# Optimization experiments

Hardware: AMD Instinct MI355X
Metric: run time of the kernel (lower is better)

The kernel has to match this reference:

```python
import jax, jax.numpy as jnp
import numpy as np

NUM_HEADS = 16

def setup_inputs() -> dict:
    key = jax.random.key(0)
    ks = jax.random.split(key, 6)
    B, S, D = 2, 2048, 1024
    x = jax.random.normal(ks[0], (B, S, D), dtype=jnp.float32)
    s = 1.0 / np.sqrt(D)
    Wq = jax.random.normal(ks[1], (D, D), dtype=jnp.float32) * s
    Wk = jax.random.normal(ks[2], (D, D), dtype=jnp.float32) * s
    Wv = jax.random.normal(ks[3], (D, D), dtype=jnp.float32) * s
    Wff = jax.random.normal(ks[4], (D, D), dtype=jnp.float32) * s
    bff = jax.random.normal(ks[5], (D,), dtype=jnp.float32) * 0.01
    return {"x": x, "Wq": Wq, "Wk": Wk, "Wv": Wv, "Wff": Wff, "bff": bff}

def reference(x, Wq, Wk, Wv, Wff, bff):
    B, S, D = x.shape
    H = NUM_HEADS
    Dh = D // H
    # Q/K/V projections (bias-free Linears). Original scales Q by 1/sqrt(hidden_size).
    q = (x @ Wq.T) * (1.0 / jnp.sqrt(jnp.asarray(D, x.dtype)))
    k = x @ Wk.T
    v = x @ Wv.T
    q = q.reshape(B, S, H, Dh)
    k = k.reshape(B, S, H, Dh)
    v = v.reshape(B, S, H, Dh)
    # Blockwise online-softmax attention is mathematically identical to
    # full softmax attention over all keys (no causal mask in source).
    scores = jnp.einsum('bqhd,bkhd->bhqk', q, k)
    attn = jax.nn.softmax(scores, axis=-1)
    out = jnp.einsum('bhqk,bkhd->bqhd', attn, v).reshape(B, S, D)
    # Final feedforward Linear(hidden, hidden) with bias.
    return out @ Wff.T + bff
```

## Files before the change

### kernel.cpp

```cpp
#include <hip/hip_runtime.h>
#include <stdint.h>

typedef __attribute__((ext_vector_type(8))) short bf16x8;
typedef __attribute__((ext_vector_type(4))) float f32x4;

__device__ __forceinline__ uint16_t f2bf(float f) {
  union { float f; uint32_t u; } a; a.f = f;
  uint32_t u = a.u;
  u += 0x7FFFu + ((u >> 16) & 1u);
  return (uint16_t)(u >> 16);
}

__device__ __forceinline__ uint32_t pk_bf16(float a, float b) {
#if __has_builtin(__builtin_amdgcn_cvt_pk_bf16_f32)
  auto r = __builtin_amdgcn_cvt_pk_bf16_f32(a, b);
  uint32_t u; __builtin_memcpy(&u, &r, sizeof(u));
  return u;
#else
  return (uint32_t)f2bf(a) | ((uint32_t)f2bf(b) << 16);
#endif
}

__device__ __forceinline__ uint32_t pk_bf16_fast(float a, float b) {
#if __has_builtin(__builtin_amdgcn_cvt_pk_bf16_f32)
  auto r = __builtin_amdgcn_cvt_pk_bf16_f32(a, b);
  uint32_t u; __builtin_memcpy(&u, &r, sizeof(u));
  return u;
#else
  uint32_t ua, ub;
  __builtin_memcpy(&ua, &a, 4); __builtin_memcpy(&ub, &b, 4);
  return __builtin_amdgcn_perm(ub, ua, 0x07060302u);
#endif
}

__device__ __forceinline__ float fast_exp2(float x) {
#if __has_builtin(__builtin_amdgcn_exp2f)
  return __builtin_amdgcn_exp2f(x);
#else
  return exp2f(x);
#endif
}

__device__ __forceinline__ void gld_lds16(const uint16_t* g, uint16_t* l) {
  __builtin_amdgcn_global_load_lds(
      (const __attribute__((address_space(1))) void*)g,
      (__attribute__((address_space(3))) void*)l, 16, 0, 0);
}

__global__ void cast_all(const float* __restrict__ x, const float* __restrict__ wq,
                         const float* __restrict__ wk, const float* __restrict__ wv,
                         const float* __restrict__ wff,
                         uint16_t* __restrict__ xb, uint16_t* __restrict__ wqb,
                         uint16_t* __restrict__ wkb, uint16_t* __restrict__ wvb,
                         uint16_t* __restrict__ wffb) {
  int i = blockIdx.x * blockDim.x + threadIdx.x;
  const float* src; uint16_t* dst; int off;
  if (i < 1048576)      { src = x;   dst = xb;   off = i; }
  else if (i < 1310720) { src = wq;  dst = wqb;  off = i - 1048576; }
  else if (i < 1572864) { src = wk;  dst = wkb;  off = i - 1310720; }
  else if (i < 1835008) { src = wv;  dst = wvb;  off = i - 1572864; }
  else                  { src = wff; dst = wffb; off = i - 1835008; }
  float4 v = ((const float4*)src)[off];
  uint2 o; o.x = pk_bf16(v.x, v.y); o.y = pk_bf16(v.z, v.w);
  ((uint2*)dst)[off] = o;
}

__device__ __forceinline__ void gemm_tile(const uint16_t* __restrict__ Abase,
                                          const uint16_t* __restrict__ Bbase,
                                          uint16_t* lds, f32x4 acc[4][4]) {
  const int tid  = threadIdx.x;
  const int w    = tid >> 6;
  const int lane = tid & 63;
  const int wm   = w >> 1, wn = w & 1;
  const int lrow = lane & 15;
  const int quad = lane >> 4;
  const int srow = lane >> 3;
  const int lc   = (lane & 7) ^ srow;
  const int sx   = lrow & 7;
  uint16_t* a_lds = lds;
  uint16_t* b_lds = lds + 8192;

#pragma unroll
  for (int mt = 0; mt < 4; ++mt)
#pragma unroll
    for (int nt = 0; nt < 4; ++nt)
      acc[mt][nt] = (f32x4){0.f, 0.f, 0.f, 0.f};

  const uint16_t* ag = Abase + (size_t)(w * 32 + srow) * 1024 + lc * 8;
  const uint16_t* bg = Bbase + (size_t)(w * 32 + srow) * 1024 + lc * 8;

  for (int k0 = 0; k0 < 1024; k0 += 64) {
#pragma unroll
    for (int i8 = 0; i8 < 4; ++i8) {
      gld_lds16(ag + (size_t)i8 * 8 * 1024 + k0, a_lds + (w * 4 + i8) * 512);
      gld_lds16(bg + (size_t)i8 * 8 * 1024 + k0, b_lds + (w * 4 + i8) * 512);
    }
    __syncthreads();
#pragma unroll
    for (int ks = 0; ks < 2; ++ks) {
      bf16x8 af[4], bfr[4];
      const int c = ((ks * 4 + quad) ^ sx) << 3;
#pragma unroll
      for (int mt = 0; mt < 4; ++mt)
        af[mt] = *(const bf16x8*)(a_lds + (wm * 64 + mt * 16 + lrow) * 64 + c);
#pragma unroll
      for (int nt = 0; nt < 4; ++nt)
        bfr[nt] = *(const bf16x8*)(b_lds + (wn * 64 + nt * 16 + lrow) * 64 + c);
#pragma unroll
      for (int mt = 0; mt < 4; ++mt)
#pragma unroll
        for (int nt = 0; nt < 4; ++nt)
          acc[mt][nt] = __builtin_amdgcn_mfma_f32_16x16x32_bf16(af[mt], bfr[nt], acc[mt][nt], 0, 0, 0);
    }
    __syncthreads();
  }
}

__global__ __launch_bounds__(256) void gemm_qkv(
    const uint16_t* __restrict__ x,
    const uint16_t* __restrict__ wq, const uint16_t* __restrict__ wk, const uint16_t* __restrict__ wv,
    uint16_t* __restrict__ qo, uint16_t* __restrict__ ko, uint16_t* __restrict__ vto) {
  __shared__ __align__(16) uint16_t lds[17408];
  const int m0 = blockIdx.x * 128, n0 = blockIdx.y * 128, z = blockIdx.z;
  f32x4 acc[4][4];
  if (z < 2) {
    const uint16_t* W = (z == 0) ? wq : wk;
    gemm_tile(W + (size_t)n0 * 1024, x + (size_t)m0 * 1024, lds, acc);
  } else {
    gemm_tile(x + (size_t)m0 * 1024, wv + (size_t)n0 * 1024, lds, acc);
  }

  const int tid = threadIdx.x;
  const int lane = tid & 63, w = tid >> 6;
  const int wm = w >> 1, wn = w & 1, lrow = lane & 15, quad = lane >> 4;
  const float scale = (z == 0) ? 0.045084222f : 1.0f;

#pragma unroll
  for (int mt = 0; mt < 4; ++mt)
#pragma unroll
    for (int nt = 0; nt < 4; ++nt) {
      int i0 = wm * 64 + mt * 16 + quad * 4;
      int j  = wn * 64 + nt * 16 + lrow;
      uint2 dd;
      dd.x = pk_bf16(acc[mt][nt][0] * scale, acc[mt][nt][1] * scale);
      dd.y = pk_bf16(acc[mt][nt][2] * scale, acc[mt][nt][3] * scale);
      *(uint2*)(&lds[j * 136 + i0]) = dd;
    }
  __syncthreads();

  uint16_t* outp = (z == 0) ? qo : (z == 1) ? ko : vto;
  if (z < 2) {
#pragma unroll
    for (int it = 0; it < 8; ++it) {
      int idx = it * 256 + tid;
      int jj = idx >> 4, cc = idx & 15;
      uint4 v = *(const uint4*)(&lds[jj * 136 + cc * 8]);
      int m = m0 + jj, n = n0 + cc * 8;
      int b = m >> 11, s = m & 2047, h = n >> 6, dh = n & 63;
      *(uint4*)(outp + ((size_t)((b * 16 + h) * 2048 + s)) * 64 + dh) = v;
    }
  } else {
    int b = m0 >> 11, sbase = m0 & 2047;
#pragma unroll
    for (int it = 0; it < 8; ++it) {
      int idx = it * 256 + tid;
      int ff = idx >> 4, cc = idx & 15;
      uint4 v = *(const uint4*)(&lds[ff * 136 + cc * 8]);
      int n = n0 + ff, h = n >> 6, dh = n & 63;
      *(uint4*)(outp + ((size_t)((b * 16 + h) * 64 + dh)) * 2048 + sbase + cc * 8) = v;
    }
  }
}

__global__ __launch_bounds__(256) void gemm_ff(
    const uint16_t* __restrict__ ao, const uint16_t* __restrict__ wff,
    const float* __restrict__ bff, float* __restrict__ out) {
  __shared__ __align__(16) uint16_t lds[17408];
  const int m0 = blockIdx.x * 128, n0 = blockIdx.y * 128;
  f32x4 acc[4][4];
  gemm_tile(wff + (size_t)n0 * 1024, ao + (size_t)m0 * 1024, lds, acc);

  const int tid = threadIdx.x;
  const int lane = tid & 63, w = tid >> 6;
  const int wm = w >> 1, wn = w & 1, lrow = lane & 15, quad = lane >> 4;
  float* fl = (float*)lds;

#pragma unroll
  for (int p = 0; p < 2; ++p) {
    if (wm == p) {
#pragma unroll
      for (int mt = 0; mt < 4; ++mt)
#pragma unroll
        for (int nt = 0; nt < 4; ++nt) {
          int i0 = mt * 16 + quad * 4;
          int j  = wn * 64 + nt * 16 + lrow;
          *(f32x4*)(&fl[j * 68 + i0]) = acc[mt][nt];
        }
    }
    __syncthreads();
#pragma unroll
    for (int it = 0; it < 8; ++it) {
      int idx = it * 256 + tid;
      int jj = idx >> 4, cc = idx & 15;
      f32x4 v = *(const f32x4*)(&fl[jj * 68 + cc * 4]);
      int n = n0 + p * 64 + cc * 4;
      f32x4 bias = *(const f32x4*)(bff + n);
      f32x4 vv = v + bias;
      *(f32x4*)(out + (size_t)(m0 + jj) * 1024 + n) = vv;
    }
    __syncthreads();
  }
}

__global__ __launch_bounds__(512, 4) void attn(
    const uint16_t* __restrict__ q, const uint16_t* __restrict__ k,
    const uint16_t* __restrict__ vt, uint16_t* __restrict__ ao) {
  __shared__ __align__(16) uint16_t lds_all[32768];
  uint16_t* const k_lds = lds_all;
  uint16_t* const v_lds = lds_all + 8192;
  uint16_t* const p_lds = lds_all + 16384;
  const int tid = threadIdx.x, w = tid >> 6, lane = tid & 63;
  const int lrow = lane & 15, quad = lane >> 4;
  const int srow = lane >> 3, lc = (lane & 7) ^ srow, sx = lrow & 7;
  const int kw = w & 3, qw = w >> 2;
  const int pk = w & 1, pq = w >> 1;
  const int pswz = (lrow & 7) << 1;

  const int lin = blockIdx.x + (blockIdx.y << 4);
  const int wl  = ((lin & 7) << 6) + (lin >> 3);
  const int qb  = wl & 15, bh = wl >> 4;

  const uint16_t* Q = q  + (size_t)bh * (2048 * 64);
  const uint16_t* K = k  + (size_t)bh * (2048 * 64);
  const uint16_t* V = vt + (size_t)bh * (64 * 2048);

  const int qr0 = qb * 128;
  bf16x8 qf[4][2];
#pragma unroll
  for (int qh = 0; qh < 4; ++qh)
#pragma unroll
    for (int ks = 0; ks < 2; ++ks)
      qf[qh][ks] = *(const bf16x8*)(Q + (size_t)(qr0 + qw * 64 + qh * 16 + lrow) * 64 + ks * 32 + quad * 8);

  f32x4 o[2][4];
#pragma unroll
  for (int qh2 = 0; qh2 < 2; ++qh2)
#pragma unroll
    for (int dt = 0; dt < 4; ++dt) o[qh2][dt] = (f32x4){0.f, 0.f, 0.f, 0.f};
  float ls[4] = {0.f, 0.f, 0.f, 0.f};
  bf16x8 vfr[4];

  auto stage = [&](int kb, int bi) {
    gld_lds16(K + (size_t)(kb * 64 + w * 8 + srow) * 64 + lc * 8, k_lds + bi * 4096 + w * 512);
    gld_lds16(V + (size_t)(w * 8 + srow) * 2048 + kb * 64 + lc * 8, v_lds + bi * 4096 + w * 512);
  };
  stage(0, 0);

  for (int kb = 0; kb < 32; ++kb) {
    const int bi = kb & 1;
    __syncthreads();

    if (kb > 0) {
      const uint16_t* pbuf = p_lds + (bi ^ 1) * 8192;
      __builtin_amdgcn_s_setprio(1);
#pragma unroll
      for (int qh2 = 0; qh2 < 2; ++qh2) {
        int row = pq * 32 + qh2 * 16 + lrow;
        bf16x8 pa = *(const bf16x8*)(pbuf + row * 64 + (((pk * 8 + quad * 2) ^ pswz) << 2));
#pragma unroll
        for (int dt = 0; dt < 4; ++dt)
          o[qh2][dt] = __builtin_amdgcn_mfma_f32_16x16x32_bf16(vfr[dt], pa, o[qh2][dt], 0, 0, 0);
      }
      __builtin_amdgcn_s_setprio(0);
    }

#pragma unroll
    for (int dt = 0; dt < 4; ++dt)
      vfr[dt] = *(const bf16x8*)(v_lds + bi * 4096 + (dt * 16 + lrow) * 64 + (((pk * 4 + quad) ^ sx) << 3));

    if (kb + 1 < 32) stage(kb + 1, bi ^ 1);

    f32x4 s[4];
#pragma unroll
    for (int qh = 0; qh < 4; ++qh) s[qh] = (f32x4){0.f, 0.f, 0.f, 0.f};
    __builtin_amdgcn_s_setprio(1);
#pragma unroll
    for (int ks = 0; ks < 2; ++ks) {
      bf16x8 kf = *(const bf16x8*)(k_lds + bi * 4096 + (kw * 16 + lrow) * 64 + (((ks * 4 + quad) ^ sx) << 3));
#pragma unroll
      for (int qh = 0; qh < 4; ++qh)
        s[qh] = __builtin_amdgcn_mfma_f32_16x16x32_bf16(kf, qf[qh][ks], s[qh], 0, 0, 0);
    }
    __builtin_amdgcn_s_setprio(0);

    uint16_t* pbw = p_lds + bi * 8192;
#pragma unroll
    for (int qh = 0; qh < 4; ++qh) {
      float p0 = fast_exp2(s[qh][0]);
      float p1 = fast_exp2(s[qh][1]);
      float p2 = fast_exp2(s[qh][2]);
      float p3 = fast_exp2(s[qh][3]);
      ls[qh] += (p0 + p1) + (p2 + p3);
      uint2 dd; dd.x = pk_bf16_fast(p0, p1); dd.y = pk_bf16_fast(p2, p3);
      int row = qw * 64 + qh * 16 + lrow;
      *(uint2*)(pbw + row * 64 + (((kw * 4 + quad) ^ pswz) << 2)) = dd;
    }
  }

  __syncthreads();
  {
    const uint16_t* pbuf = p_lds + 8192;
    __builtin_amdgcn_s_setprio(1);
#pragma unroll
    for (int qh2 = 0; qh2 < 2; ++qh2) {
      int row = pq * 32 + qh2 * 16 + lrow;
      bf16x8 pa = *(const bf16x8*)(pbuf + row * 64 + (((pk * 8 + quad * 2) ^ pswz) << 2));
#pragma unroll
      for (int dt = 0; dt < 4; ++dt)
        o[qh2][dt] = __builtin_amdgcn_mfma_f32_16x16x32_bf16(vfr[dt], pa, o[qh2][dt], 0, 0, 0);
    }
    __builtin_amdgcn_s_setprio(0);
  }
  __syncthreads();

#pragma unroll
  for (int qh = 0; qh < 4; ++qh) {
    ls[qh] += __shfl_xor(ls[qh], 16);
    ls[qh] += __shfl_xor(ls[qh], 32);
  }
  float* arena = (float*)lds_all;
  float* lred  = (float*)(lds_all + 17408);
  if (quad == 0) {
#pragma unroll
    for (int qh = 0; qh < 4; ++qh) lred[kw * 128 + qw * 64 + qh * 16 + lrow] = ls[qh];
  }
  if (pk == 1) {
#pragma unroll
    for (int qh2 = 0; qh2 < 2; ++qh2)
#pragma unroll
      for (int dt = 0; dt < 4; ++dt)
        *(f32x4*)(&arena[(pq * 32 + qh2 * 16 + lrow) * 68 + dt * 16 + quad * 4]) = o[qh2][dt];
  }
  __syncthreads();

  if (pk == 0) {
    const int b = bh >> 4, h = bh & 15;
#pragma unroll
    for (int qh2 = 0; qh2 < 2; ++qh2) {
      int qrow = pq * 32 + qh2 * 16 + lrow;
      float l = lred[qrow] + lred[128 + qrow] + lred[256 + qrow] + lred[384 + qrow];
      float inv = 1.0f / l;
      int sg = qr0 + qrow;
#pragma unroll
      for (int dt = 0; dt < 4; ++dt) {
        f32x4 a = *(const f32x4*)(&arena[qrow * 68 + dt * 16 + quad * 4]);
        uint2 dd;
        dd.x = pk_bf16((o[qh2][dt][0] + a[0]) * inv, (o[qh2][dt][1] + a[1]) * inv);
        dd.y = pk_bf16((o[qh2][dt][2] + a[2]) * inv, (o[qh2][dt][3] + a[3]) * inv);
        *(uint2*)(ao + (size_t)(b * 2048 + sg) * 1024 + h * 64 + dt * 16 + quad * 4) = dd;
      }
    }
  }
}

extern "C" void kernel_launch(void* const* d_in, const int* in_sizes, int n_in,
                              void* d_out, int out_size, void* d_ws, size_t ws_size,
                              hipStream_t stream) {
  const float* x   = (const float*)d_in[0];
  const float* Wq  = (const float*)d_in[1];
  const float* Wk  = (const float*)d_in[2];
  const float* Wv  = (const float*)d_in[3];
  const float* Wff = (const float*)d_in[4];
  const float* bff = (const float*)d_in[5];
  float* out = (float*)d_out;

  uint16_t* ws = (uint16_t*)d_ws;
  uint16_t* x_bf   = ws;
  uint16_t* wq_bf  = ws + 4194304;
  uint16_t* wk_bf  = ws + 5242880;
  uint16_t* wv_bf  = ws + 6291456;
  uint16_t* wff_bf = ws + 7340032;
  uint16_t* q_bf   = ws + 8388608;
  uint16_t* k_bf   = ws + 12582912;
  uint16_t* vt_bf  = ws + 16777216;
  uint16_t* ao_bf  = ws + 20971520;

  cast_all<<<8192, 256, 0, stream>>>(x, Wq, Wk, Wv, Wff, x_bf, wq_bf, wk_bf, wv_bf, wff_bf);

  gemm_qkv<<<dim3(32, 8, 3), 256, 0, stream>>>(x_bf, wq_bf, wk_bf, wv_bf, q_bf, k_bf, vt_bf);
  attn<<<dim3(16, 32), 512, 0, stream>>>(q_bf, k_bf, vt_bf, ao_bf);
  gemm_ff<<<dim3(32, 8), 256, 0, stream>>>(ao_bf, wff_bf, bff, out);
}
```

Measured before the change: 176.6 us.

## Halve gemm_ff N-tile to double grid size and swizzle M-block order

The feedforward GEMM moves from 128x128 to 128x64 output tiles using its own inlined K loop, which doubles the grid from 256 to 512 workgroups. This is meant to fill the 256 CUs of the device more evenly. Both gemm_qkv and gemm_ff also remap blockIdx.x with an interleaving swizzle so that blocks running at the same time touch different M rows, aiming for better cache locality. The cost is that each block loads more of A relative to its output, lowering arithmetic intensity, and each wave issues fewer MFMAs per LDS load.

```diff
diff --git a/kernel.cpp b/kernel.cpp
--- a/kernel.cpp
+++ b/kernel.cpp
@@ -121,7 +121,9 @@
     const uint16_t* __restrict__ wq, const uint16_t* __restrict__ wk, const uint16_t* __restrict__ wv,
     uint16_t* __restrict__ qo, uint16_t* __restrict__ ko, uint16_t* __restrict__ vto) {
   __shared__ __align__(16) uint16_t lds[17408];
-  const int m0 = blockIdx.x * 128, n0 = blockIdx.y * 128, z = blockIdx.z;
+  const int bx = blockIdx.x;
+  const int mi = ((bx & 7) << 2) + (bx >> 3);
+  const int m0 = mi * 128, n0 = blockIdx.y * 128, z = blockIdx.z;
   f32x4 acc[4][4];
   if (z < 2) {
     const uint16_t* W = (z == 0) ? wq : wk;
@@ -175,38 +177,79 @@
 __global__ __launch_bounds__(256) void gemm_ff(
     const uint16_t* __restrict__ ao, const uint16_t* __restrict__ wff,
     const float* __restrict__ bff, float* __restrict__ out) {
-  __shared__ __align__(16) uint16_t lds[17408];
-  const int m0 = blockIdx.x * 128, n0 = blockIdx.y * 128;
-  f32x4 acc[4][4];
-  gemm_tile(wff + (size_t)n0 * 1024, ao + (size_t)m0 * 1024, lds, acc);
-
-  const int tid = threadIdx.x;
-  const int lane = tid & 63, w = tid >> 6;
-  const int wm = w >> 1, wn = w & 1, lrow = lane & 15, quad = lane >> 4;
+  __shared__ __align__(16) uint16_t lds[12288];
+  const int bx = blockIdx.x;
+  const int mi = ((bx & 7) << 2) + (bx >> 3);
+  const int m0 = mi * 128, n0 = blockIdx.y * 64;
+  const int tid  = threadIdx.x;
+  const int w    = tid >> 6;
+  const int lane = tid & 63;
+  const int wm   = w >> 1, wn = w & 1;
+  const int lrow = lane & 15;
+  const int quad = lane >> 4;
+  const int srow = lane >> 3;
+  const int lc   = (lane & 7) ^ srow;
+  const int sx   = lrow & 7;
+  uint16_t* a_lds = lds;
+  uint16_t* b_lds = lds + 4096;
+
+  f32x4 acc[4][2];
+#pragma unroll
+  for (int mt = 0; mt < 4; ++mt)
+#pragma unroll
+    for (int nt = 0; nt < 2; ++nt)
+      acc[mt][nt] = (f32x4){0.f, 0.f, 0.f, 0.f};
+
+  const uint16_t* ag = wff + (size_t)(n0 + w * 16 + srow) * 1024 + lc * 8;
+  const uint16_t* bg = ao  + (size_t)(m0 + w * 32 + srow) * 1024 + lc * 8;
+
+  for (int k0 = 0; k0 < 1024; k0 += 64) {
+#pragma unroll
+    for (int i2 = 0; i2 < 2; ++i2)
+      gld_lds16(ag + (size_t)i2 * 8 * 1024 + k0, a_lds + (w * 2 + i2) * 512);
+#pragma unroll
+    for (int i8 = 0; i8 < 4; ++i8)
+      gld_lds16(bg + (size_t)i8 * 8 * 1024 + k0, b_lds + (w * 4 + i8) * 512);
+    __syncthreads();
+#pragma unroll
+    for (int ks = 0; ks < 2; ++ks) {
+      bf16x8 af[2], bfr[4];
+      const int c = ((ks * 4 + quad) ^ sx) << 3;
+#pragma unroll
+      for (int nt = 0; nt < 2; ++nt)
+        af[nt] = *(const bf16x8*)(a_lds + (wn * 32 + nt * 16 + lrow) * 64 + c);
+#pragma unroll
+      for (int mt = 0; mt < 4; ++mt)
+        bfr[mt] = *(const bf16x8*)(b_lds + (wm * 64 + mt * 16 + lrow) * 64 + c);
+#pragma unroll
+      for (int mt = 0; mt < 4; ++mt)
+#pragma unroll
+        for (int nt = 0; nt < 2; ++nt)
+          acc[mt][nt] = __builtin_amdgcn_mfma_f32_16x16x32_bf16(af[nt], bfr[mt], acc[mt][nt], 0, 0, 0);
+    }
+    __syncthreads();
+  }
+
   float* fl = (float*)lds;
-
 #pragma unroll
   for (int p = 0; p < 2; ++p) {
     if (wm == p) {
 #pragma unroll
       for (int mt = 0; mt < 4; ++mt)
 #pragma unroll
-        for (int nt = 0; nt < 4; ++nt) {
-          int i0 = mt * 16 + quad * 4;
-          int j  = wn * 64 + nt * 16 + lrow;
-          *(f32x4*)(&fl[j * 68 + i0]) = acc[mt][nt];
-        }
-    }
-    __syncthreads();
-#pragma unroll
-    for (int it = 0; it < 8; ++it) {
+        for (int nt = 0; nt < 2; ++nt)
+          *(f32x4*)(&fl[(mt * 16 + lrow) * 68 + wn * 32 + nt * 16 + quad * 4]) = acc[mt][nt];
+    }
+    __syncthreads();
+#pragma unroll
+    for (int it = 0; it < 4; ++it) {
       int idx = it * 256 + tid;
       int jj = idx >> 4, cc = idx & 15;
       f32x4 v = *(const f32x4*)(&fl[jj * 68 + cc * 4]);
-      int n = n0 + p * 64 + cc * 4;
+      int n = n0 + cc * 4;
       f32x4 bias = *(const f32x4*)(bff + n);
       f32x4 vv = v + bias;
-      *(f32x4*)(out + (size_t)(m0 + jj) * 1024 + n) = vv;
+      *(f32x4*)(out + (size_t)(m0 + p * 64 + jj) * 1024 + n) = vv;
     }
     __syncthreads();
   }
@@ -389,5 +432,5 @@
 
   gemm_qkv<<<dim3(32, 8, 3), 256, 0, stream>>>(x_bf, wq_bf, wk_bf, wv_bf, q_bf, k_bf, vt_bf);
   attn<<<dim3(16, 32), 512, 0, stream>>>(q_bf, k_bf, vt_bf, ao_bf);
-  gemm_ff<<<dim3(32, 8), 256, 0, stream>>>(ao_bf, wff_bf, bff, out);
-}
+  gemm_ff<<<dim3(32, 16), 256, 0, stream>>>(ao_bf, wff_bf, bff, out);
+}
```

Measured after the change: 173.7 us (median of 2 runs). About the same (-1.7%).
